# Kernel tuning notes

Hardware: AMD Instinct MI355X
Metric: run time of the kernel (lower is better)

Reference implementation:

```python
import jax, jax.numpy as jnp
import numpy as np

EMBED = 1024

def setup_inputs() -> dict:
    key = jax.random.key(0)
    ks = jax.random.split(key, 7)
    s = 1.0 / np.sqrt(EMBED)  # ~ torch Linear default init scale
    x = jax.random.normal(ks[0], (4, 2048, EMBED), dtype=jnp.float32)
    Wq = jax.random.uniform(ks[1], (EMBED, EMBED), jnp.float32, -s, s)
    bq = jax.random.uniform(ks[2], (EMBED,), jnp.float32, -s, s)
    Wk = jax.random.uniform(ks[3], (EMBED, EMBED), jnp.float32, -s, s)
    bk = jax.random.uniform(ks[4], (EMBED,), jnp.float32, -s, s)
    Wv = jax.random.uniform(ks[5], (EMBED, EMBED), jnp.float32, -s, s)
    bv = jax.random.uniform(ks[6], (EMBED,), jnp.float32, -s, s)
    return {"x": x, "Wq": Wq, "bq": bq, "Wk": Wk, "bk": bk, "Wv": Wv, "bv": bv}

def reference(x, Wq, bq, Wk, bk, Wv, bv):
    # torch nn.Linear: y = x @ W.T + b
    q = jnp.einsum('bse,oe->bso', x, Wq) + bq
    k = jnp.einsum('bse,oe->bso', x, Wk) + bk
    v = jnp.einsum('bse,oe->bso', x, Wv) + bv
    scale = 1.0 / jnp.sqrt(jnp.float32(x.shape[-1]))
    scores = jnp.einsum('bqd,bkd->bqk', q, k) * scale  # [B,S,S]
    weights = jax.nn.softmax(scores, axis=-1)
    return jnp.einsum('bqk,bkd->bqd', weights, v)
```

## Files before the change

kernel.cpp:

```cpp
#include <hip/hip_runtime.h>
#include <stdint.h>

#define B_   4
#define S_   2048
#define E_   1024
#define MQKV (B_ * S_)
#define LDQ  1056
#define LDP  2112

typedef __bf16 bf16x8 __attribute__((ext_vector_type(8)));
typedef float f32x4 __attribute__((ext_vector_type(4)));
typedef unsigned short u16;
typedef unsigned int u32;

__device__ __forceinline__ u16 f2bf(float x) {
  union { float f; u32 u; } c; c.f = x;
  u32 r = (c.u + 0x7FFFu + ((c.u >> 16) & 1u)) >> 16;
  return (u16)r;
}
__device__ __forceinline__ float bf2f(u16 h) {
  union { u32 u; float f; } c; c.u = ((u32)h) << 16;
  return c.f;
}

__global__ __launch_bounds__(256) void cvt_all(
    const float* __restrict__ x, const float* __restrict__ wq,
    const float* __restrict__ wk, const float* __restrict__ wv,
    u16* __restrict__ dst) {
  const int gid = blockIdx.x * 256 + threadIdx.x;
  const int total = 2097152 + 786432;
  const int stride = gridDim.x * 256;
  for (int i = gid; i < total; i += stride) {
    float4 f;
    if (i < 2097152) {
      f = reinterpret_cast<const float4*>(x)[i];
    } else {
      const int j = i - 2097152;
      const int sel = j >> 18;
      const int r = j & 262143;
      const float* s = sel == 0 ? wq : (sel == 1 ? wk : wv);
      f = reinterpret_cast<const float4*>(s)[r];
    }
    ushort4 o;
    o.x = f2bf(f.x); o.y = f2bf(f.y); o.z = f2bf(f.z); o.w = f2bf(f.w);
    reinterpret_cast<ushort4*>(dst)[i] = o;
  }
}

#define GLOAD_LDS16(g, l)                                                      \
  __builtin_amdgcn_global_load_lds(                                            \
      (const __attribute__((address_space(1))) u32*)(g),                       \
      (__attribute__((address_space(3))) u32*)(l), 16, 0, 0)

template <int BN, int EPI>
__device__ __forceinline__ void gemm_body(
    const u16* __restrict__ A, const u16* __restrict__ Bt, void* __restrict__ Cv,
    const float* __restrict__ b0, const float* __restrict__ b1,
    int N, int K, float scale,
    long sA, long sB, long sC, long ldA, long ldB, long ldC, int gx, int gy) {
  constexpr int BM = 256;
  constexpr int NR = BN / 64;
  constexpr int L  = 2 + BN / 128;
  constexpr int BSLOT = BN * 32;

  __shared__ alignas(16) u16 lds[4 * BM * 32 + 4 * BSLOT];
  u16* lA = lds;
  u16* lB = lds + 4 * BM * 32;

  const int t = threadIdx.x;
  const int wv = t >> 6;
  const int ln = t & 63;
  const int wm = wv >> 2;
  const int wn = wv & 3;

  const int nwg = gridDim.x;
  int id = blockIdx.x;
  id = (id & 7) * (nwg >> 3) + (id >> 3);
  const int pz = gx * gy;
  const int z = id / pz;
  const int r2 = id - z * pz;
  const int by = r2 / gx;
  const int bx = r2 - by * gx;
  const int bm = by * BM;
  const int bn = bx * BN;

  A += (size_t)z * sA;
  Bt += (size_t)z * sB;

  const int srow = t >> 2;
  const int g0 = (t & 3) ^ ((srow >> 1) & 3);
  const u16* gA0 = A + (size_t)(bm + srow) * ldA + g0 * 8;
  const u16* gA1 = gA0 + (size_t)128 * ldA;
  const u16* gB0 = Bt + (size_t)(bn + srow) * ldB + g0 * 8;
  const u16* gB1 = gB0 + (size_t)128 * ldB;

  auto STAGE = [&](int u) {
    const int s = u & 3;
    const int ko = u * 32;
    GLOAD_LDS16(gA0 + ko, lA + s * 8192 + wv * 512);
    GLOAD_LDS16(gA1 + ko, lA + s * 8192 + 4096 + wv * 512);
    GLOAD_LDS16(gB0 + ko, lB + s * BSLOT + wv * 512);
    if constexpr (BN == 256) GLOAD_LDS16(gB1 + ko, lB + s * BSLOT + 4096 + wv * 512);
  };

  const int lrow = ln & 15;
  const int g = ln >> 4;
  const int aR = wm * 128 + lrow;
  const int aOff = aR * 32 + (g ^ ((aR >> 1) & 3)) * 8;
  const int bR = wn * (BN / 4) + lrow;
  const int bOff = bR * 32 + (g ^ ((bR >> 1) & 3)) * 8;

  f32x4 acc[8][NR] = {};
  const int T = K >> 5;

  bf16x8 afA[8], afB[8], bgA[NR], bgB[NR];

#define RD_A(DST, TILE) do { const u16* _p = lA + ((TILE) & 3) * 8192 + aOff;  \
  _Pragma("unroll") for (int _i = 0; _i < 8; ++_i)                             \
    DST[_i] = *reinterpret_cast<const bf16x8*>(_p + _i * 512); } while (0)
#define RD_B(DST, TILE) do { const u16* _p = lB + ((TILE) & 3) * BSLOT + bOff; \
  _Pragma("unroll") for (int _j = 0; _j < NR; ++_j)                            \
    DST[_j] = *reinterpret_cast<const bf16x8*>(_p + _j * 512); } while (0)
#define DO_MFMA(AF, BG) do { __builtin_amdgcn_s_setprio(1);                    \
  _Pragma("unroll") for (int _i = 0; _i < 8; ++_i)                             \
  _Pragma("unroll") for (int _j = 0; _j < NR; ++_j)                            \
    acc[_i][_j] = __builtin_amdgcn_mfma_f32_16x16x32_bf16(AF[_i], BG[_j],      \
                                                          acc[_i][_j], 0, 0, 0);\
  __builtin_amdgcn_s_setprio(0); } while (0)
#define VM_GATE(COND) do {                                                     \
  if (COND) { asm volatile("s_waitcnt vmcnt(%0)" :: "n"(L) : "memory"); }      \
  else { asm volatile("s_waitcnt vmcnt(0)" ::: "memory"); }                    \
  __builtin_amdgcn_s_barrier(); asm volatile("" ::: "memory"); } while (0)

  STAGE(0); STAGE(1); STAGE(2);
  asm volatile("s_waitcnt vmcnt(%0)" :: "n"(L) : "memory");
  __builtin_amdgcn_s_barrier();
  asm volatile("" ::: "memory");

  if constexpr (NR == 2) { RD_A(afA, 0); RD_B(bgA, 0); }
  else                   { RD_B(bgA, 0); }

  for (int tt = 0; tt < T; tt += 2) {
    if (tt + 3 < T) STAGE(tt + 3);
    if constexpr (NR == 2) { RD_A(afB, tt + 1); RD_B(bgB, tt + 1); DO_MFMA(afA, bgA); }
    else                   { RD_A(afA, tt); RD_B(bgB, tt + 1);     DO_MFMA(afA, bgA); }
    VM_GATE(tt + 3 < T);

    if (tt + 4 < T) STAGE(tt + 4);
    if constexpr (NR == 2) {
      if (tt + 2 < T) { RD_A(afA, tt + 2); RD_B(bgA, tt + 2); }
      DO_MFMA(afB, bgB);
    } else {
      RD_A(afA, tt + 1);
      if (tt + 2 < T) RD_B(bgA, tt + 2);
      DO_MFMA(afA, bgB);
    }
    VM_GATE(tt + 4 < T);
  }
#undef RD_A
#undef RD_B
#undef DO_MFMA
#undef VM_GATE

  const int r0 = (ln >> 4) * 4;
  const int c0 = ln & 15;
#pragma unroll
  for (int i = 0; i < 8; ++i) {
#pragma unroll
    for (int j = 0; j < NR; ++j) {
      const int col = bn + wn * (BN / 4) + j * 16 + c0;
#pragma unroll
      for (int ii = 0; ii < 4; ++ii) {
        const int row = bm + wm * 128 + i * 16 + r0 + ii;
        float v = acc[i][j][ii];
        if constexpr (EPI == 0) {
          const int sel = col >> 10;
          const int cc = col & 1023;
          const float bb = sel == 0 ? b0[cc] : b1[cc];
          ((u16*)Cv)[(size_t)sel * 8650752 + (size_t)row * LDQ + cc] = f2bf(v + bb);
        } else if constexpr (EPI == 1) {
          ((u16*)Cv)[(size_t)z * sC + (size_t)row * ldC + col] = f2bf(v + b0[row]);
        } else {
          ((u16*)Cv)[(size_t)z * sC + (size_t)row * ldC + col] = f2bf(__expf(v * scale));
        }
      }
    }
  }
}

__global__ __launch_bounds__(512, 2) void qkproj_k(
    const u16* __restrict__ A, const u16* __restrict__ Bt, void* __restrict__ Cv,
    const float* __restrict__ b0, const float* __restrict__ b1,
    int N, int K, float scale, long sA, long sB, long sC,
    long ldA, long ldB, long ldC, int gx, int gy) {
  gemm_body<256, 0>(A, Bt, Cv, b0, b1, N, K, scale, sA, sB, sC, ldA, ldB, ldC, gx, gy);
}
__global__ __launch_bounds__(512, 2) void vproj_k(
    const u16* __restrict__ A, const u16* __restrict__ Bt, void* __restrict__ Cv,
    const float* __restrict__ b0, const float* __restrict__ b1,
    int N, int K, float scale, long sA, long sB, long sC,
    long ldA, long ldB, long ldC, int gx, int gy) {
  gemm_body<128, 1>(A, Bt, Cv, b0, b1, N, K, scale, sA, sB, sC, ldA, ldB, ldC, gx, gy);
}
__global__ __launch_bounds__(512, 2) void qkt_k(
    const u16* __restrict__ A, const u16* __restrict__ Bt, void* __restrict__ Cv,
    const float* __restrict__ b0, const float* __restrict__ b1,
    int N, int K, float scale, long sA, long sB, long sC,
    long ldA, long ldB, long ldC, int gx, int gy) {
  gemm_body<256, 2>(A, Bt, Cv, b0, b1, N, K, scale, sA, sB, sC, ldA, ldB, ldC, gx, gy);
}

__global__ __launch_bounds__(256) void row_invsum(const u16* __restrict__ P,
                                                  float* __restrict__ invL) {
  const int row = blockIdx.x * 4 + (threadIdx.x >> 6);
  const int ln = threadIdx.x & 63;
  const u16* p = P + (size_t)row * LDP + ln * 32;
  float s = 0.f;
#pragma unroll
  for (int q = 0; q < 4; ++q) {
    uint4 r = reinterpret_cast<const uint4*>(p)[q];
    u32 w[4] = {r.x, r.y, r.z, r.w};
#pragma unroll
    for (int k = 0; k < 4; ++k) {
      s += bf2f((u16)(w[k] & 0xffffu));
      s += bf2f((u16)(w[k] >> 16));
    }
  }
  for (int o = 1; o < 64; o <<= 1) s += __shfl_xor(s, o);
  if (ln == 0) invL[row] = 1.0f / s;
}

__global__ __launch_bounds__(512, 2) void pv_k(
    const u16* __restrict__ Pm, const u16* __restrict__ vt,
    float* __restrict__ out, const float* __restrict__ invL) {
  __shared__ alignas(16) u16 lA[3 * 16384];
  __shared__ alignas(16) u16 lB[3 * 8192];
  const int t = threadIdx.x;
  const int wv = t >> 6, ln = t & 63;
  const int wm = wv >> 2, wn = wv & 3;

  int id = blockIdx.x;
  id = (id & 7) * 32 + (id >> 3);
  const int z = id >> 6;
  const int r2 = id & 63;
  const int by = r2 >> 3, bx = r2 & 7;
  const int bm = by * 256, bn = bx * 128;

  const u16* A = Pm + (size_t)z * 2048 * LDP;
  const u16* Bt = vt + (size_t)z * 1024 * LDP;

  const int sr = t >> 3;
  const int scw = ((t & 7) ^ (sr & 7)) * 8;
  const u16* Ab = A + (size_t)(bm + sr) * LDP + scw;
  const u16* Bb = Bt + (size_t)(bn + sr) * LDP + scw;

#define PSTG(u) do { const int _s = (u) % 3; const long _ko = (long)(u) * 64;  \
  _Pragma("unroll") for (int _q = 0; _q < 4; ++_q)                             \
    GLOAD_LDS16(Ab + (size_t)_q * 64 * LDP + _ko, lA + _s * 16384 + _q * 4096 + t * 8); \
  _Pragma("unroll") for (int _q = 0; _q < 2; ++_q)                             \
    GLOAD_LDS16(Bb + (size_t)_q * 64 * LDP + _ko, lB + _s * 8192 + _q * 4096 + t * 8);  \
} while (0)

  const int lrow = ln & 15, g = ln >> 4;
  const int ch0 = (g ^ (lrow & 7)) * 8;
  const int ch1 = ((4 | g) ^ (lrow & 7)) * 8;

  f32x4 acc[8][2] = {};

  PSTG(0); PSTG(1);
  asm volatile("s_waitcnt vmcnt(6)" ::: "memory");
  __builtin_amdgcn_s_barrier();
  asm volatile("" ::: "memory");

  for (int u = 0; u < 32; ++u) {
    if (u + 2 < 32) PSTG(u + 2);
    const int s = u % 3;
    const u16* pA = lA + s * 16384 + lrow * 64;
    const u16* pB = lB + s * 8192 + lrow * 64;
    bf16x8 a[8][2], b[2][2];
#pragma unroll
    for (int mf = 0; mf < 8; ++mf) {
      const int ro = (wm * 128 + mf * 16) * 64;
      a[mf][0] = *reinterpret_cast<const bf16x8*>(pA + ro + ch0);
      a[mf][1] = *reinterpret_cast<const bf16x8*>(pA + ro + ch1);
    }
#pragma unroll
    for (int nf = 0; nf < 2; ++nf) {
      const int ro = (wn * 32 + nf * 16) * 64;
      b[nf][0] = *reinterpret_cast<const bf16x8*>(pB + ro + ch0);
      b[nf][1] = *reinterpret_cast<const bf16x8*>(pB + ro + ch1);
    }
    __builtin_amdgcn_s_setprio(1);
#pragma unroll
    for (int ks = 0; ks < 2; ++ks)
#pragma unroll
      for (int mf = 0; mf < 8; ++mf)
#pragma unroll
        for (int nf = 0; nf < 2; ++nf)
          acc[mf][nf] = __builtin_amdgcn_mfma_f32_16x16x32_bf16(
              a[mf][ks], b[nf][ks], acc[mf][nf], 0, 0, 0);
    __builtin_amdgcn_s_setprio(0);
    if (u < 31) {
      if (u + 2 < 32) { asm volatile("s_waitcnt vmcnt(6)" ::: "memory"); }
      else            { asm volatile("s_waitcnt vmcnt(0)" ::: "memory"); }
      __builtin_amdgcn_s_barrier();
      asm volatile("" ::: "memory");
    }
  }
#undef PSTG

  const int r0 = g * 4, c0 = lrow;
#pragma unroll
  for (int mf = 0; mf < 8; ++mf) {
#pragma unroll
    for (int ii = 0; ii < 4; ++ii) {
      const int row = bm + wm * 128 + mf * 16 + r0 + ii;
      const float inv = invL[z * 2048 + row];
#pragma unroll
      for (int nf = 0; nf < 2; ++nf) {
        const int col = bn + wn * 32 + nf * 16 + c0;
        out[((size_t)z * 2048 + row) * 1024 + col] = acc[mf][nf][ii] * inv;
      }
    }
  }
}

extern "C" void kernel_launch(void* const* d_in, const int* in_sizes, int n_in,
                              void* d_out, int out_size, void* d_ws, size_t ws_size,
                              hipStream_t stream) {
  const float* x = (const float*)d_in[0];
  const float* Wq = (const float*)d_in[1];
  const float* bq = (const float*)d_in[2];
  const float* Wk = (const float*)d_in[3];
  const float* bk = (const float*)d_in[4];
  const float* Wv = (const float*)d_in[5];
  const float* bv = (const float*)d_in[6];
  float* out = (float*)d_out;

  const size_t xE = 8388608, wE = 3145728;
  const size_t qE = (size_t)8192 * LDQ;
  const size_t vtE = (size_t)4 * 1024 * LDP;
  const size_t PmE = (size_t)4 * 2048 * LDP;
  const size_t need = (xE + wE + 2 * qE + vtE + PmE) * 2 + (size_t)MQKV * 4;
  if (ws_size < need) {
    hipMemsetAsync(d_out, 0, (size_t)out_size * sizeof(float), stream);
    return;
  }
  u16* xb = (u16*)d_ws;
  u16* wqkv = xb + xE;
  u16* qb = wqkv + wE;
  u16* vt = qb + 2 * qE;
  u16* Pm = vt + vtE;
  float* invL = (float*)(Pm + PmE);

  cvt_all<<<2048, 256, 0, stream>>>(x, Wq, Wk, Wv, xb);

  qkproj_k<<<256, 512, 0, stream>>>(
      xb, wqkv, qb, bq, bk, 2048, E_, 1.f,
      0, 0, 0, E_, E_, LDQ, 8, 32);

  vproj_k<<<256, 512, 0, stream>>>(
      wqkv + 2 * (size_t)E_ * E_, xb, vt, bv, nullptr, 2048, E_, 1.f,
      0, (long)S_ * E_, (long)1024 * LDP, E_, E_, LDP, 16, 4);

  qkt_k<<<256, 512, 0, stream>>>(
      qb, qb + qE, Pm, nullptr, nullptr, 2048, E_, 0.03125f,
      (long)S_ * LDQ, (long)S_ * LDQ, (long)2048 * LDP, LDQ, LDQ, LDP, 8, 8);

  row_invsum<<<B_ * S_ / 4, 256, 0, stream>>>(Pm, invL);

  pv_k<<<256, 512, 0, stream>>>(Pm, vt, out, invL);
}
```

Measured before the change: 160.5 us.

## Rewrite 256x256 GEMMs with BK=64 double-buffer and 8-phase load/MFMA interleave

The QK projection and QK^T GEMMs move to a new body with a 64-wide K step, two 64KB LDS buffers, an 8-column XOR swizzle, and an 8-phase schedule. In that schedule each quarter-tile of MFMAs is interleaved with issuing part of the next tile's global-to-LDS loads. The V projection keeps the old 4-stage BK=32 pipeline in a specialised standalone kernel. The aim is better overlap of memory traffic with MFMA work and fewer waits per K step. In exchange it uses more barriers per tile and larger LDS (128KB), which may limit occupancy to one block per CU.

```diff
diff --git a/kernel.cpp b/kernel.cpp
--- a/kernel.cpp
+++ b/kernel.cpp
@@ -7,6 +7,7 @@
 #define MQKV (B_ * S_)
 #define LDQ  1056
 #define LDP  2112
+#define QOFF 8650752
 
 typedef __bf16 bf16x8 __attribute__((ext_vector_type(8)));
 typedef float f32x4 __attribute__((ext_vector_type(4)));
@@ -52,26 +53,17 @@
       (const __attribute__((address_space(1))) u32*)(g),                       \
       (__attribute__((address_space(3))) u32*)(l), 16, 0, 0)
 
-template <int BN, int EPI>
-__device__ __forceinline__ void gemm_body(
+template <int EPI>
+__device__ __forceinline__ void g8p_body(
     const u16* __restrict__ A, const u16* __restrict__ Bt, void* __restrict__ Cv,
     const float* __restrict__ b0, const float* __restrict__ b1,
-    int N, int K, float scale,
-    long sA, long sB, long sC, long ldA, long ldB, long ldC, int gx, int gy) {
-  constexpr int BM = 256;
-  constexpr int NR = BN / 64;
-  constexpr int L  = 2 + BN / 128;
-  constexpr int BSLOT = BN * 32;
-
-  __shared__ alignas(16) u16 lds[4 * BM * 32 + 4 * BSLOT];
-  u16* lA = lds;
-  u16* lB = lds + 4 * BM * 32;
+    int K, float scale, long sA, long sB, long sC,
+    long ldA, long ldB, long ldC, int gx, int gy) {
+  __shared__ alignas(16) u16 lds[65536];
 
   const int t = threadIdx.x;
-  const int wv = t >> 6;
-  const int ln = t & 63;
-  const int wm = wv >> 2;
-  const int wn = wv & 3;
+  const int wv = t >> 6, ln = t & 63;
+  const int wm = wv >> 2, wn = wv & 3;
 
   const int nwg = gridDim.x;
   int id = blockIdx.x;
@@ -81,18 +73,149 @@
   const int r2 = id - z * pz;
   const int by = r2 / gx;
   const int bx = r2 - by * gx;
-  const int bm = by * BM;
-  const int bn = bx * BN;
+  const int bm = by * 256, bn = bx * 256;
 
   A += (size_t)z * sA;
   Bt += (size_t)z * sB;
 
+  const int sr = t >> 3;
+  const int scw = ((t & 7) ^ (sr & 7)) * 8;
+  const u16* Ab = A + (size_t)(bm + sr) * ldA + scw;
+  const u16* Bb = Bt + (size_t)(bn + sr) * ldB + scw;
+
+#define SA_(BUF, H, KT) do { const long _ko = (long)(KT) * 64;                 \
+    GLOAD_LDS16(Ab + (size_t)(H) * 64 * ldA + _ko,                             \
+                lds + (BUF) * 32768 + (H) * 4096 + t * 8);                     \
+    GLOAD_LDS16(Ab + (size_t)(2 + (H)) * 64 * ldA + _ko,                       \
+                lds + (BUF) * 32768 + (2 + (H)) * 4096 + t * 8); } while (0)
+#define SB_(BUF, H, KT) do { const long _ko = (long)(KT) * 64;                 \
+    GLOAD_LDS16(Bb + (size_t)(2 * (H)) * 64 * ldB + _ko,                       \
+                lds + (BUF) * 32768 + 16384 + 2 * (H) * 4096 + t * 8);         \
+    GLOAD_LDS16(Bb + (size_t)(2 * (H) + 1) * 64 * ldB + _ko,                   \
+                lds + (BUF) * 32768 + 16384 + (2 * (H) + 1) * 4096 + t * 8); } while (0)
+
+  const int lrow = ln & 15, g = ln >> 4;
+  const int chX0 = (g ^ (lrow & 7)) * 8;
+  const int chX1 = ((4 | g) ^ (lrow & 7)) * 8;
+
+  f32x4 acc[8][4] = {};
+  const int NT = K >> 6;
+
+#define PHASE(BUF, MH, NH, VM, ...) do {                                       \
+    bf16x8 a_[4][2], b_[2][2];                                                 \
+    const u16* _ba = lds + (BUF) * 32768 + (wm * 2 + (MH)) * 4096 + lrow * 64; \
+    const u16* _bb = lds + (BUF) * 32768 + 16384 + wn * 4096 + lrow * 64;      \
+    _Pragma("unroll") for (int _m = 0; _m < 4; ++_m) {                         \
+      a_[_m][0] = *reinterpret_cast<const bf16x8*>(_ba + _m * 1024 + chX0);    \
+      a_[_m][1] = *reinterpret_cast<const bf16x8*>(_ba + _m * 1024 + chX1);    \
+    }                                                                          \
+    _Pragma("unroll") for (int _n = 0; _n < 2; ++_n) {                         \
+      b_[_n][0] = *reinterpret_cast<const bf16x8*>(_bb + ((NH)*2+_n)*1024 + chX0);\
+      b_[_n][1] = *reinterpret_cast<const bf16x8*>(_bb + ((NH)*2+_n)*1024 + chX1);\
+    }                                                                          \
+    __builtin_amdgcn_s_barrier();                                              \
+    asm volatile("" ::: "memory");                                             \
+    __VA_ARGS__;                                                               \
+    __builtin_amdgcn_s_setprio(1);                                             \
+    _Pragma("unroll") for (int _ks = 0; _ks < 2; ++_ks)                        \
+    _Pragma("unroll") for (int _m = 0; _m < 4; ++_m)                           \
+    _Pragma("unroll") for (int _n = 0; _n < 2; ++_n)                           \
+      acc[(MH)*4+_m][(NH)*2+_n] = __builtin_amdgcn_mfma_f32_16x16x32_bf16(     \
+          a_[_m][_ks], b_[_n][_ks], acc[(MH)*4+_m][(NH)*2+_n], 0, 0, 0);       \
+    __builtin_amdgcn_s_setprio(0);                                             \
+    if (VM) asm volatile("s_waitcnt vmcnt(4)" ::: "memory");                   \
+    __builtin_amdgcn_s_barrier();                                              \
+    asm volatile("" ::: "memory");                                             \
+  } while (0)
+
+  SA_(0, 0, 0); SA_(0, 1, 0);
+  SB_(0, 0, 0); SB_(0, 1, 0);
+  SA_(1, 0, 1); SA_(1, 1, 1);
+  asm volatile("s_waitcnt vmcnt(4)" ::: "memory");
+  __builtin_amdgcn_s_barrier();
+  asm volatile("" ::: "memory");
+
+  for (int it = 0; it < (NT >> 1); ++it) {
+    const int T0 = 2 * it;
+    const bool g2 = (T0 + 2) < NT;
+    const bool g3 = (T0 + 3) < NT;
+    PHASE(0, 0, 0, false, { SB_(1, 0, T0 + 1); SB_(1, 1, T0 + 1); });
+    PHASE(0, 0, 1, false, {});
+    PHASE(0, 1, 0, false, { if (g2) SA_(0, 0, T0 + 2); });
+    PHASE(0, 1, 1, true,  { if (g2) SA_(0, 1, T0 + 2); });
+    PHASE(1, 0, 0, false, { if (g2) { SB_(0, 0, T0 + 2); SB_(0, 1, T0 + 2); } });
+    PHASE(1, 0, 1, false, {});
+    PHASE(1, 1, 0, false, { if (g3) SA_(1, 0, T0 + 3); });
+    PHASE(1, 1, 1, true,  { if (g3) SA_(1, 1, T0 + 3); });
+  }
+#undef PHASE
+#undef SA_
+#undef SB_
+
+  const int r0 = g * 4, c0 = lrow;
+#pragma unroll
+  for (int mf = 0; mf < 8; ++mf) {
+#pragma unroll
+    for (int ii = 0; ii < 4; ++ii) {
+      const int row = bm + wm * 128 + mf * 16 + r0 + ii;
+#pragma unroll
+      for (int nf = 0; nf < 4; ++nf) {
+        const int col = bn + wn * 64 + nf * 16 + c0;
+        const float v = acc[mf][nf][ii];
+        if constexpr (EPI == 0) {
+          const int sel = col >> 10;
+          const int cc = col & 1023;
+          const float bb = sel == 0 ? b0[cc] : b1[cc];
+          ((u16*)Cv)[(size_t)sel * QOFF + (size_t)row * LDQ + cc] = f2bf(v + bb);
+        } else {
+          ((u16*)Cv)[(size_t)z * sC + (size_t)row * ldC + col] = f2bf(__expf(v * scale));
+        }
+      }
+    }
+  }
+}
+
+__global__ __launch_bounds__(512, 2) void qkproj_k(
+    const u16* __restrict__ A, const u16* __restrict__ Bt, void* __restrict__ Cv,
+    const float* __restrict__ b0, const float* __restrict__ b1,
+    int K, float scale, long sA, long sB, long sC,
+    long ldA, long ldB, long ldC, int gx, int gy) {
+  g8p_body<0>(A, Bt, Cv, b0, b1, K, scale, sA, sB, sC, ldA, ldB, ldC, gx, gy);
+}
+__global__ __launch_bounds__(512, 2) void qkt_k(
+    const u16* __restrict__ A, const u16* __restrict__ Bt, void* __restrict__ Cv,
+    const float* __restrict__ b0, const float* __restrict__ b1,
+    int K, float scale, long sA, long sB, long sC,
+    long ldA, long ldB, long ldC, int gx, int gy) {
+  g8p_body<2>(A, Bt, Cv, b0, b1, K, scale, sA, sB, sC, ldA, ldB, ldC, gx, gy);
+}
+
+__global__ __launch_bounds__(512, 2) void vproj_k(
+    const u16* __restrict__ A, const u16* __restrict__ Bt, void* __restrict__ Cv,
+    const float* __restrict__ b0,
+    int K, long sB, long sC, long ldA, long ldB, long ldC, int gx, int gy) {
+  constexpr int BN = 128, BM = 256, NR = 2, L = 3, BSLOT = BN * 32;
+  __shared__ alignas(16) u16 lds[4 * BM * 32 + 4 * BSLOT];
+  u16* lA = lds;
+  u16* lB = lds + 4 * BM * 32;
+  const int t = threadIdx.x;
+  const int wv = t >> 6, ln = t & 63;
+  const int wm = wv >> 2, wn = wv & 3;
+  const int nwg = gridDim.x;
+  int id = blockIdx.x;
+  id = (id & 7) * (nwg >> 3) + (id >> 3);
+  const int pz = gx * gy;
+  const int z = id / pz;
+  const int r2 = id - z * pz;
+  const int by = r2 / gx;
+  const int bx = r2 - by * gx;
+  const int bm = by * BM, bn = bx * BN;
+  Bt += (size_t)z * sB;
   const int srow = t >> 2;
   const int g0 = (t & 3) ^ ((srow >> 1) & 3);
   const u16* gA0 = A + (size_t)(bm + srow) * ldA + g0 * 8;
   const u16* gA1 = gA0 + (size_t)128 * ldA;
   const u16* gB0 = Bt + (size_t)(bn + srow) * ldB + g0 * 8;
-  const u16* gB1 = gB0 + (size_t)128 * ldB;
 
   auto STAGE = [&](int u) {
     const int s = u & 3;
@@ -100,21 +223,15 @@
     GLOAD_LDS16(gA0 + ko, lA + s * 8192 + wv * 512);
     GLOAD_LDS16(gA1 + ko, lA + s * 8192 + 4096 + wv * 512);
     GLOAD_LDS16(gB0 + ko, lB + s * BSLOT + wv * 512);
-    if constexpr (BN == 256) GLOAD_LDS16(gB1 + ko, lB + s * BSLOT + 4096 + wv * 512);
   };
-
-  const int lrow = ln & 15;
-  const int g = ln >> 4;
+  const int lrow = ln & 15, g = ln >> 4;
   const int aR = wm * 128 + lrow;
   const int aOff = aR * 32 + (g ^ ((aR >> 1) & 3)) * 8;
   const int bR = wn * (BN / 4) + lrow;
   const int bOff = bR * 32 + (g ^ ((bR >> 1) & 3)) * 8;
-
   f32x4 acc[8][NR] = {};
   const int T = K >> 5;
-
   bf16x8 afA[8], afB[8], bgA[NR], bgB[NR];
-
 #define RD_A(DST, TILE) do { const u16* _p = lA + ((TILE) & 3) * 8192 + aOff;  \
   _Pragma("unroll") for (int _i = 0; _i < 8; ++_i)                             \
     DST[_i] = *reinterpret_cast<const bf16x8*>(_p + _i * 512); } while (0)
@@ -131,37 +248,24 @@
   if (COND) { asm volatile("s_waitcnt vmcnt(%0)" :: "n"(L) : "memory"); }      \
   else { asm volatile("s_waitcnt vmcnt(0)" ::: "memory"); }                    \
   __builtin_amdgcn_s_barrier(); asm volatile("" ::: "memory"); } while (0)
-
   STAGE(0); STAGE(1); STAGE(2);
   asm volatile("s_waitcnt vmcnt(%0)" :: "n"(L) : "memory");
   __builtin_amdgcn_s_barrier();
   asm volatile("" ::: "memory");
-
-  if constexpr (NR == 2) { RD_A(afA, 0); RD_B(bgA, 0); }
-  else                   { RD_B(bgA, 0); }
-
+  RD_A(afA, 0); RD_B(bgA, 0);
   for (int tt = 0; tt < T; tt += 2) {
     if (tt + 3 < T) STAGE(tt + 3);
-    if constexpr (NR == 2) { RD_A(afB, tt + 1); RD_B(bgB, tt + 1); DO_MFMA(afA, bgA); }
-    else                   { RD_A(afA, tt); RD_B(bgB, tt + 1);     DO_MFMA(afA, bgA); }
+    RD_A(afB, tt + 1); RD_B(bgB, tt + 1); DO_MFMA(afA, bgA);
     VM_GATE(tt + 3 < T);
-
     if (tt + 4 < T) STAGE(tt + 4);
-    if constexpr (NR == 2) {
-      if (tt + 2 < T) { RD_A(afA, tt + 2); RD_B(bgA, tt + 2); }
-      DO_MFMA(afB, bgB);
-    } else {
-      RD_A(afA, tt + 1);
-      if (tt + 2 < T) RD_B(bgA, tt + 2);
-      DO_MFMA(afA, bgB);
-    }
+    if (tt + 2 < T) { RD_A(afA, tt + 2); RD_B(bgA, tt + 2); }
+    DO_MFMA(afB, bgB);
     VM_GATE(tt + 4 < T);
   }
 #undef RD_A
 #undef RD_B
 #undef DO_MFMA
 #undef VM_GATE
-
   const int r0 = (ln >> 4) * 4;
   const int c0 = ln & 15;
 #pragma unroll
@@ -172,42 +276,11 @@
 #pragma unroll
       for (int ii = 0; ii < 4; ++ii) {
         const int row = bm + wm * 128 + i * 16 + r0 + ii;
-        float v = acc[i][j][ii];
-        if constexpr (EPI == 0) {
-          const int sel = col >> 10;
-          const int cc = col & 1023;
-          const float bb = sel == 0 ? b0[cc] : b1[cc];
-          ((u16*)Cv)[(size_t)sel * 8650752 + (size_t)row * LDQ + cc] = f2bf(v + bb);
-        } else if constexpr (EPI == 1) {
-          ((u16*)Cv)[(size_t)z * sC + (size_t)row * ldC + col] = f2bf(v + b0[row]);
-        } else {
-          ((u16*)Cv)[(size_t)z * sC + (size_t)row * ldC + col] = f2bf(__expf(v * scale));
-        }
+        ((u16*)Cv)[(size_t)z * sC + (size_t)row * ldC + col] =
+            f2bf(acc[i][j][ii] + b0[row]);
       }
     }
   }
-}
-
-__global__ __launch_bounds__(512, 2) void qkproj_k(
-    const u16* __restrict__ A, const u16* __restrict__ Bt, void* __restrict__ Cv,
-    const float* __restrict__ b0, const float* __restrict__ b1,
-    int N, int K, float scale, long sA, long sB, long sC,
-    long ldA, long ldB, long ldC, int gx, int gy) {
-  gemm_body<256, 0>(A, Bt, Cv, b0, b1, N, K, scale, sA, sB, sC, ldA, ldB, ldC, gx, gy);
-}
-__global__ __launch_bounds__(512, 2) void vproj_k(
-    const u16* __restrict__ A, const u16* __restrict__ Bt, void* __restrict__ Cv,
-    const float* __restrict__ b0, const float* __restrict__ b1,
-    int N, int K, float scale, long sA, long sB, long sC,
-    long ldA, long ldB, long ldC, int gx, int gy) {
-  gemm_body<128, 1>(A, Bt, Cv, b0, b1, N, K, scale, sA, sB, sC, ldA, ldB, ldC, gx, gy);
-}
-__global__ __launch_bounds__(512, 2) void qkt_k(
-    const u16* __restrict__ A, const u16* __restrict__ Bt, void* __restrict__ Cv,
-    const float* __restrict__ b0, const float* __restrict__ b1,
-    int N, int K, float scale, long sA, long sB, long sC,
-    long ldA, long ldB, long ldC, int gx, int gy) {
-  gemm_body<256, 2>(A, Bt, Cv, b0, b1, N, K, scale, sA, sB, sC, ldA, ldB, ldC, gx, gy);
 }
 
 __global__ __launch_bounds__(256) void row_invsum(const u16* __restrict__ P,
@@ -356,15 +429,15 @@
   cvt_all<<<2048, 256, 0, stream>>>(x, Wq, Wk, Wv, xb);
 
   qkproj_k<<<256, 512, 0, stream>>>(
-      xb, wqkv, qb, bq, bk, 2048, E_, 1.f,
+      xb, wqkv, qb, bq, bk, E_, 1.f,
       0, 0, 0, E_, E_, LDQ, 8, 32);
 
   vproj_k<<<256, 512, 0, stream>>>(
-      wqkv + 2 * (size_t)E_ * E_, xb, vt, bv, nullptr, 2048, E_, 1.f,
-      0, (long)S_ * E_, (long)1024 * LDP, E_, E_, LDP, 16, 4);
+      wqkv + 2 * (size_t)E_ * E_, xb, vt, bv, E_,
+      (long)S_ * E_, (long)1024 * LDP, E_, E_, LDP, 16, 4);
 
   qkt_k<<<256, 512, 0, stream>>>(
-      qb, qb + qE, Pm, nullptr, nullptr, 2048, E_, 0.03125f,
+      qb, qb + QOFF, Pm, nullptr, nullptr, E_, 0.03125f,
       (long)S_ * LDQ, (long)S_ * LDQ, (long)2048 * LDP, LDQ, LDQ, LDP, 8, 8);
 
   row_invsum<<<B_ * S_ / 4, 256, 0, stream>>>(Pm, invL);
```

Result: slower. 168.4 us (+4.9%).

## Use 128x128 double-buffered GEMM tiles for QK^T and PV kernels

Applied to the files above, without the earlier changes.

Replaces the 256-row, 512-thread tiled QK^T and PV kernels with a shared 128x128-tile, 256-thread, double-buffered GEMM body. This yields 1024 and 512 workgroups instead of 256, to improve occupancy and load balance across CUs. The cost is less data reuse per tile (more global/LDS traffic per FLOP) and a different pipelining depth (2 stages instead of 3 for PV).

```diff
diff --git a/kernel.cpp b/kernel.cpp
--- a/kernel.cpp
+++ b/kernel.cpp
@@ -7,6 +7,7 @@
 #define MQKV (B_ * S_)
 #define LDQ  1056
 #define LDP  2112
+#define QOFF 8650752
 
 typedef __bf16 bf16x8 __attribute__((ext_vector_type(8)));
 typedef float f32x4 __attribute__((ext_vector_type(4)));
@@ -177,11 +178,9 @@
           const int sel = col >> 10;
           const int cc = col & 1023;
           const float bb = sel == 0 ? b0[cc] : b1[cc];
-          ((u16*)Cv)[(size_t)sel * 8650752 + (size_t)row * LDQ + cc] = f2bf(v + bb);
-        } else if constexpr (EPI == 1) {
+          ((u16*)Cv)[(size_t)sel * QOFF + (size_t)row * LDQ + cc] = f2bf(v + bb);
+        } else {
           ((u16*)Cv)[(size_t)z * sC + (size_t)row * ldC + col] = f2bf(v + b0[row]);
-        } else {
-          ((u16*)Cv)[(size_t)z * sC + (size_t)row * ldC + col] = f2bf(__expf(v * scale));
         }
       }
     }
@@ -202,12 +201,123 @@
     long ldA, long ldB, long ldC, int gx, int gy) {
   gemm_body<128, 1>(A, Bt, Cv, b0, b1, N, K, scale, sA, sB, sC, ldA, ldB, ldC, gx, gy);
 }
-__global__ __launch_bounds__(512, 2) void qkt_k(
-    const u16* __restrict__ A, const u16* __restrict__ Bt, void* __restrict__ Cv,
-    const float* __restrict__ b0, const float* __restrict__ b1,
-    int N, int K, float scale, long sA, long sB, long sC,
-    long ldA, long ldB, long ldC, int gx, int gy) {
-  gemm_body<256, 2>(A, Bt, Cv, b0, b1, N, K, scale, sA, sB, sC, ldA, ldB, ldC, gx, gy);
+
+template <int EPI>
+__device__ __forceinline__ void g128_body(
+    const u16* __restrict__ A, const u16* __restrict__ Bt, void* __restrict__ Cv,
+    const float* __restrict__ b0,
+    int K, float scale, long sA, long sB, long sC,
+    long ldA, long ldB, long ldC, int gx, int gy) {
+  __shared__ alignas(16) u16 lA[2 * 8192];
+  __shared__ alignas(16) u16 lB[2 * 8192];
+  const int t = threadIdx.x;
+  const int wv = t >> 6, ln = t & 63;
+  const int wm = wv >> 1, wn = wv & 1;
+
+  const int nwg = gridDim.x;
+  int id = blockIdx.x;
+  id = (id & 7) * (nwg >> 3) + (id >> 3);
+  const int pz = gx * gy;
+  const int z = id / pz;
+  const int r2 = id - z * pz;
+  const int by = r2 / gx;
+  const int bx = r2 - by * gx;
+  const int bm = by * 128, bn = bx * 128;
+
+  A += (size_t)z * sA;
+  Bt += (size_t)z * sB;
+
+  const int sr = t >> 3;
+  const int scw = ((t & 7) ^ (sr & 7)) * 8;
+  const u16* Ab = A + (size_t)(bm + sr) * ldA + scw;
+  const u16* Bb = Bt + (size_t)(bn + sr) * ldB + scw;
+
+#define STG(u) do { const int _s = ((u) & 1) * 8192; const long _ko = (long)(u) * 64; \
+  _Pragma("unroll") for (int _q = 0; _q < 4; ++_q) {                           \
+    GLOAD_LDS16(Ab + (size_t)(_q * 32) * ldA + _ko, lA + _s + _q * 2048 + t * 8); \
+    GLOAD_LDS16(Bb + (size_t)(_q * 32) * ldB + _ko, lB + _s + _q * 2048 + t * 8); } \
+} while (0)
+
+  const int lrow = ln & 15, g = ln >> 4;
+  const int ch0 = (g ^ (lrow & 7)) * 8;
+  const int ch1 = ((4 | g) ^ (lrow & 7)) * 8;
+
+  f32x4 acc[4][4] = {};
+  const int T = K >> 6;
+
+  STG(0);
+  for (int u = 0; u < T; ++u) {
+    if (u + 1 < T) {
+      STG(u + 1);
+      asm volatile("s_waitcnt vmcnt(8)" ::: "memory");
+    } else {
+      asm volatile("s_waitcnt vmcnt(0)" ::: "memory");
+    }
+    __builtin_amdgcn_s_barrier();
+    asm volatile("" ::: "memory");
+
+    const int s = (u & 1) * 8192;
+    const u16* pA = lA + s + (wm * 64 + lrow) * 64;
+    const u16* pB = lB + s + (wn * 64 + lrow) * 64;
+    bf16x8 a[4][2], b[4][2];
+#pragma unroll
+    for (int mf = 0; mf < 4; ++mf) {
+      a[mf][0] = *reinterpret_cast<const bf16x8*>(pA + mf * 1024 + ch0);
+      a[mf][1] = *reinterpret_cast<const bf16x8*>(pA + mf * 1024 + ch1);
+    }
+#pragma unroll
+    for (int nf = 0; nf < 4; ++nf) {
+      b[nf][0] = *reinterpret_cast<const bf16x8*>(pB + nf * 1024 + ch0);
+      b[nf][1] = *reinterpret_cast<const bf16x8*>(pB + nf * 1024 + ch1);
+    }
+    __builtin_amdgcn_s_setprio(1);
+#pragma unroll
+    for (int ks = 0; ks < 2; ++ks)
+#pragma unroll
+      for (int mf = 0; mf < 4; ++mf)
+#pragma unroll
+        for (int nf = 0; nf < 4; ++nf)
+          acc[mf][nf] = __builtin_amdgcn_mfma_f32_16x16x32_bf16(
+              a[mf][ks], b[nf][ks], acc[mf][nf], 0, 0, 0);
+    __builtin_amdgcn_s_setprio(0);
+    __builtin_amdgcn_s_barrier();
+    asm volatile("" ::: "memory");
+  }
+#undef STG
+
+  const int r0 = g * 4, c0 = lrow;
+#pragma unroll
+  for (int mf = 0; mf < 4; ++mf) {
+#pragma unroll
+    for (int ii = 0; ii < 4; ++ii) {
+      const int row = bm + wm * 64 + mf * 16 + r0 + ii;
+#pragma unroll
+      for (int nf = 0; nf < 4; ++nf) {
+        const int col = bn + wn * 64 + nf * 16 + c0;
+        const float v = acc[mf][nf][ii];
+        if constexpr (EPI == 2) {
+          ((u16*)Cv)[(size_t)z * sC + (size_t)row * ldC + col] = f2bf(__expf(v * scale));
+        } else {
+          ((float*)Cv)[(size_t)z * sC + (size_t)row * ldC + col] = v * b0[z * 2048 + row];
+        }
+      }
+    }
+  }
+}
+
+__global__ __launch_bounds__(256) void qkt_k(
+    const u16* __restrict__ A, const u16* __restrict__ Bt, void* __restrict__ Cv,
+    const float* __restrict__ b0,
+    int K, float scale, long sA, long sB, long sC,
+    long ldA, long ldB, long ldC, int gx, int gy) {
+  g128_body<2>(A, Bt, Cv, b0, K, scale, sA, sB, sC, ldA, ldB, ldC, gx, gy);
+}
+__global__ __launch_bounds__(256) void pv_k(
+    const u16* __restrict__ A, const u16* __restrict__ Bt, void* __restrict__ Cv,
+    const float* __restrict__ b0,
+    int K, float scale, long sA, long sB, long sC,
+    long ldA, long ldB, long ldC, int gx, int gy) {
+  g128_body<3>(A, Bt, Cv, b0, K, scale, sA, sB, sC, ldA, ldB, ldC, gx, gy);
 }
 
 __global__ __launch_bounds__(256) void row_invsum(const u16* __restrict__ P,
@@ -228,101 +338,6 @@
   }
   for (int o = 1; o < 64; o <<= 1) s += __shfl_xor(s, o);
   if (ln == 0) invL[row] = 1.0f / s;
-}
-
-__global__ __launch_bounds__(512, 2) void pv_k(
-    const u16* __restrict__ Pm, const u16* __restrict__ vt,
-    float* __restrict__ out, const float* __restrict__ invL) {
-  __shared__ alignas(16) u16 lA[3 * 16384];
-  __shared__ alignas(16) u16 lB[3 * 8192];
-  const int t = threadIdx.x;
-  const int wv = t >> 6, ln = t & 63;
-  const int wm = wv >> 2, wn = wv & 3;
-
-  int id = blockIdx.x;
-  id = (id & 7) * 32 + (id >> 3);
-  const int z = id >> 6;
-  const int r2 = id & 63;
-  const int by = r2 >> 3, bx = r2 & 7;
-  const int bm = by * 256, bn = bx * 128;
-
-  const u16* A = Pm + (size_t)z * 2048 * LDP;
-  const u16* Bt = vt + (size_t)z * 1024 * LDP;
-
-  const int sr = t >> 3;
-  const int scw = ((t & 7) ^ (sr & 7)) * 8;
-  const u16* Ab = A + (size_t)(bm + sr) * LDP + scw;
-  const u16* Bb = Bt + (size_t)(bn + sr) * LDP + scw;
-
-#define PSTG(u) do { const int _s = (u) % 3; const long _ko = (long)(u) * 64;  \
-  _Pragma("unroll") for (int _q = 0; _q < 4; ++_q)                             \
-    GLOAD_LDS16(Ab + (size_t)_q * 64 * LDP + _ko, lA + _s * 16384 + _q * 4096 + t * 8); \
-  _Pragma("unroll") for (int _q = 0; _q < 2; ++_q)                             \
-    GLOAD_LDS16(Bb + (size_t)_q * 64 * LDP + _ko, lB + _s * 8192 + _q * 4096 + t * 8);  \
-} while (0)
-
-  const int lrow = ln & 15, g = ln >> 4;
-  const int ch0 = (g ^ (lrow & 7)) * 8;
-  const int ch1 = ((4 | g) ^ (lrow & 7)) * 8;
-
-  f32x4 acc[8][2] = {};
-
-  PSTG(0); PSTG(1);
-  asm volatile("s_waitcnt vmcnt(6)" ::: "memory");
-  __builtin_amdgcn_s_barrier();
-  asm volatile("" ::: "memory");
-
-  for (int u = 0; u < 32; ++u) {
-    if (u + 2 < 32) PSTG(u + 2);
-    const int s = u % 3;
-    const u16* pA = lA + s * 16384 + lrow * 64;
-    const u16* pB = lB + s * 8192 + lrow * 64;
-    bf16x8 a[8][2], b[2][2];
-#pragma unroll
-    for (int mf = 0; mf < 8; ++mf) {
-      const int ro = (wm * 128 + mf * 16) * 64;
-      a[mf][0] = *reinterpret_cast<const bf16x8*>(pA + ro + ch0);
-      a[mf][1] = *reinterpret_cast<const bf16x8*>(pA + ro + ch1);
-    }
-#pragma unroll
-    for (int nf = 0; nf < 2; ++nf) {
-      const int ro = (wn * 32 + nf * 16) * 64;
-      b[nf][0] = *reinterpret_cast<const bf16x8*>(pB + ro + ch0);
-      b[nf][1] = *reinterpret_cast<const bf16x8*>(pB + ro + ch1);
-    }
-    __builtin_amdgcn_s_setprio(1);
-#pragma unroll
-    for (int ks = 0; ks < 2; ++ks)
-#pragma unroll
-      for (int mf = 0; mf < 8; ++mf)
-#pragma unroll
-        for (int nf = 0; nf < 2; ++nf)
-          acc[mf][nf] = __builtin_amdgcn_mfma_f32_16x16x32_bf16(
-              a[mf][ks], b[nf][ks], acc[mf][nf], 0, 0, 0);
-    __builtin_amdgcn_s_setprio(0);
-    if (u < 31) {
-      if (u + 2 < 32) { asm volatile("s_waitcnt vmcnt(6)" ::: "memory"); }
-      else            { asm volatile("s_waitcnt vmcnt(0)" ::: "memory"); }
-      __builtin_amdgcn_s_barrier();
-      asm volatile("" ::: "memory");
-    }
-  }
-#undef PSTG
-
-  const int r0 = g * 4, c0 = lrow;
-#pragma unroll
-  for (int mf = 0; mf < 8; ++mf) {
-#pragma unroll
-    for (int ii = 0; ii < 4; ++ii) {
-      const int row = bm + wm * 128 + mf * 16 + r0 + ii;
-      const float inv = invL[z * 2048 + row];
-#pragma unroll
-      for (int nf = 0; nf < 2; ++nf) {
-        const int col = bn + wn * 32 + nf * 16 + c0;
-        out[((size_t)z * 2048 + row) * 1024 + col] = acc[mf][nf][ii] * inv;
-      }
-    }
-  }
 }
 
 extern "C" void kernel_launch(void* const* d_in, const int* in_sizes, int n_in,
@@ -363,11 +378,13 @@
       wqkv + 2 * (size_t)E_ * E_, xb, vt, bv, nullptr, 2048, E_, 1.f,
       0, (long)S_ * E_, (long)1024 * LDP, E_, E_, LDP, 16, 4);
 
-  qkt_k<<<256, 512, 0, stream>>>(
-      qb, qb + qE, Pm, nullptr, nullptr, 2048, E_, 0.03125f,
-      (long)S_ * LDQ, (long)S_ * LDQ, (long)2048 * LDP, LDQ, LDQ, LDP, 8, 8);
+  qkt_k<<<1024, 256, 0, stream>>>(
+      qb, qb + QOFF, Pm, nullptr, E_, 0.03125f,
+      (long)S_ * LDQ, (long)S_ * LDQ, (long)2048 * LDP, LDQ, LDQ, LDP, 16, 16);
 
   row_invsum<<<B_ * S_ / 4, 256, 0, stream>>>(Pm, invL);
 
-  pv_k<<<256, 512, 0, stream>>>(Pm, vt, out, invL);
-}
+  pv_k<<<512, 256, 0, stream>>>(
+      Pm, vt, out, invL, S_, 1.f,
+      (long)2048 * LDP, (long)1024 * LDP, (long)S_ * E_, LDP, LDP, 1024, 8, 16);
+}
```

New measurement: 164.6 us. +2.5%, slower.
